# Performance work log

Measured on AMD Instinct MI355X. Metric: run time of the kernel, lower is better.

Reference implementation:

```python
import jax, jax.numpy as jnp
import numpy as np

EPS = 1e-5

def conv3x3(x, w, bias=None):
    y = jax.lax.conv_general_dilated(x, w, (1, 1), 'SAME',
                                     dimension_numbers=('NCHW', 'OIHW', 'NCHW'))
    if bias is not None:
        y = y + bias[None, :, None, None]
    return y

def batchnorm(x, g, b):
    m = x.mean((0, 2, 3), keepdims=True)
    v = x.var((0, 2, 3), keepdims=True)
    return (x - m) * jax.lax.rsqrt(v + EPS) * g[None, :, None, None] + b[None, :, None, None]

def deform_sample(x, offset, mask, dg=2):
    # x: [B,C,H,W]; offset: [B,dg*9*2,H,W] (dy,dx interleaved per mmcv); mask: [B,dg*9,H,W]
    B, C, H, W = x.shape
    K = 9
    cg = C // dg
    off = offset.reshape(B, dg, K, 2, H, W)
    dy, dx = off[:, :, :, 0], off[:, :, :, 1]
    m = mask.reshape(B, dg, K, H, W)
    ky = (jnp.repeat(jnp.arange(3), 3) - 1).astype(x.dtype)   # kernel row offset per tap
    kx = (jnp.tile(jnp.arange(3), 3) - 1).astype(x.dtype)     # kernel col offset per tap
    py = dy + jnp.arange(H, dtype=x.dtype)[None, None, None, :, None] + ky[None, None, :, None, None]
    px = dx + jnp.arange(W, dtype=x.dtype)[None, None, None, None, :] + kx[None, None, :, None, None]
    y0 = jnp.floor(py); x0 = jnp.floor(px)
    ly = py - y0; lx = px - x0
    y0i = y0.astype(jnp.int32); x0i = x0.astype(jnp.int32)
    y1i = y0i + 1; x1i = x0i + 1
    def ok(yy, xx):
        return ((yy >= 0) & (yy < H) & (xx >= 0) & (xx < W)).astype(x.dtype)
    xg = x.reshape(B, dg, cg, H * W)
    def gather(yy, xx):
        idx = (jnp.clip(yy, 0, H - 1) * W + jnp.clip(xx, 0, W - 1)).reshape(B, dg, -1)
        g = jax.vmap(jax.vmap(lambda im, ii: im[:, ii]))(xg, idx)   # [B,dg,cg,K*H*W]
        return g.reshape(B, dg, cg, K, H, W)
    w00 = ((1 - ly) * (1 - lx) * ok(y0i, x0i))[:, :, None]
    w01 = ((1 - ly) * lx * ok(y0i, x1i))[:, :, None]
    w10 = (ly * (1 - lx) * ok(y1i, x0i))[:, :, None]
    w11 = (ly * lx * ok(y1i, x1i))[:, :, None]
    val = (gather(y0i, x0i) * w00 + gather(y0i, x1i) * w01 +
           gather(y1i, x0i) * w10 + gather(y1i, x1i) * w11)
    return val * m[:, :, None]   # [B,dg,cg,K,H,W]

def reference(input_v, input_i, off_w, off_b, dconv_w, bn1_g, bn1_b, conv2_w, bn2_g, bn2_b):
    x = jnp.concatenate([input_v, input_i], axis=1)             # [B,C,H,W]
    off_all = conv3x3(x, off_w, off_b)                          # [B,54,H,W]
    o1, o2, mask = jnp.split(off_all, 3, axis=1)
    offset = jnp.concatenate([o1, o2], axis=1)                  # [B,36,H,W]
    mask = jax.nn.sigmoid(mask)                                 # [B,18,H,W]
    sampled = deform_sample(x, offset, mask, dg=2)              # [B,2,cg,9,H,W]
    O = dconv_w.shape[0]
    out = jnp.einsum('bgckhw,ogck->bohw', sampled, dconv_w.reshape(O, 2, -1, 9))
    out = jax.nn.relu(batchnorm(out, bn1_g, bn1_b))
    out = jax.nn.relu(batchnorm(conv3x3(out, conv2_w), bn2_g, bn2_b))
    return out

def setup_inputs() -> dict:
    key = jax.random.key(0)
    ks = jax.random.split(key, 8)
    B, Cm, O, H, W = 4, 128, 128, 64, 64
    C = 2 * Cm
    inp = {}
    inp['input_v'] = jax.random.normal(ks[0], (B, Cm, H, W), jnp.float32)
    inp['input_i'] = jax.random.normal(ks[1], (B, Cm, H, W), jnp.float32)
    # offset/mask conv (zero-init in torch; small random here for a non-trivial reference)
    inp['off_w'] = jax.random.normal(ks[2], (54, C, 3, 3), jnp.float32) * 0.02
    inp['off_b'] = jnp.zeros((54,), jnp.float32)
    inp['dconv_w'] = jax.random.normal(ks[3], (O, C, 3, 3), jnp.float32) * (1.0 / np.sqrt(C * 9))
    inp['bn1_g'] = jnp.ones((O,), jnp.float32)
    inp['bn1_b'] = jnp.zeros((O,), jnp.float32)
    inp['conv2_w'] = jax.random.normal(ks[4], (O, O, 3, 3), jnp.float32) * (1.0 / np.sqrt(O * 9))
    inp['bn2_g'] = jnp.ones((O,), jnp.float32)
    inp['bn2_b'] = jnp.zeros((O,), jnp.float32)
    return inp
```

## Files before the change

### kernel.cpp

```cpp
#include <hip/hip_runtime.h>

#define EPSBN 1e-5f

using s8v = __attribute__((ext_vector_type(8))) short;
using f4v = __attribute__((ext_vector_type(4))) float;

__device__ inline unsigned short f2bf(float f) {
  unsigned u = __float_as_uint(f);
  return (unsigned short)((u + 0x7FFFu + ((u >> 16) & 1u)) >> 16);
}
__device__ inline float bf2f(unsigned short h) {
  return __uint_as_float(((unsigned)h) << 16);
}

__global__ __launch_bounds__(256) void k_pack(const float* __restrict__ v, const float* __restrict__ im,
                                              unsigned short* __restrict__ xb) {
  __shared__ float tile[64][33];
  int b = blockIdx.z;
  int hw0 = blockIdx.x * 32;
  int c0 = blockIdx.y * 64;
  int tx = threadIdx.x, ty = threadIdx.y;
#pragma unroll
  for (int i = 0; i < 64; i += 8) {
    int c = c0 + ty + i;
    const float* src = (c < 128) ? (v + ((size_t)b * 128 + c) * 4096)
                                 : (im + ((size_t)b * 128 + (c - 128)) * 4096);
    tile[ty + i][tx] = src[hw0 + tx];
  }
  __syncthreads();
#pragma unroll
  for (int i = 0; i < 32; i += 8) {
    int hw = hw0 + ty + i;
    ushort2 o;
    o.x = f2bf(tile[2 * tx][ty + i]);
    o.y = f2bf(tile[2 * tx + 1][ty + i]);
    *(ushort2*)&xb[((size_t)(b * 4096 + hw)) * 256 + c0 + 2 * tx] = o;
  }
}

__global__ __launch_bounds__(256) void k_wprep_off(const float* __restrict__ w, unsigned short* __restrict__ wt) {
  int id = blockIdx.x * 256 + threadIdx.x;
  int lane = id & 63;
  int nb = (id >> 6) & 3;
  int ks = id >> 8;
  int ks2 = ks & 1, tap = (ks >> 1) % 9, cc = ks / 18;
  int o = nb * 16 + (lane & 15);
  int cb = cc * 64 + ks2 * 32 + ((lane >> 4) * 8);
  s8v r;
#pragma unroll
  for (int j = 0; j < 8; ++j) {
    float val = (o < 54) ? w[((size_t)o * 256 + cb + j) * 9 + tap] : 0.f;
    r[j] = (short)f2bf(val);
  }
  *(s8v*)&wt[(size_t)id * 8] = r;
}
__global__ __launch_bounds__(256) void k_wprep_d(const float* __restrict__ w, unsigned short* __restrict__ wt) {
  int id = blockIdx.x * 256 + threadIdx.x;
  int lane = id & 63;
  int nb = (id >> 6) & 7;
  int kstep = id >> 9;
  int chunk = kstep >> 2, ks4 = kstep & 3;
  int g = chunk / 9, kk = chunk % 9;
  int o = nb * 16 + (lane & 15);
  int cb = g * 128 + ks4 * 32 + ((lane >> 4) * 8);
  s8v r;
#pragma unroll
  for (int j = 0; j < 8; ++j) r[j] = (short)f2bf(w[((size_t)o * 256 + cb + j) * 9 + kk]);
  *(s8v*)&wt[(size_t)id * 8] = r;
}
__global__ __launch_bounds__(256) void k_wprep_2(const float* __restrict__ w, unsigned short* __restrict__ wt) {
  int id = blockIdx.x * 256 + threadIdx.x;
  int lane = id & 63;
  int nb = (id >> 6) & 7;
  int kstep = id >> 9;
  int ks2 = kstep & 1, tap = (kstep >> 1) % 9, cc = kstep / 18;
  int o = nb * 16 + (lane & 15);
  int cb = cc * 64 + ks2 * 32 + ((lane >> 4) * 8);
  s8v r;
#pragma unroll
  for (int j = 0; j < 8; ++j) r[j] = (short)f2bf(w[((size_t)o * 128 + cb + j) * 9 + tap]);
  *(s8v*)&wt[(size_t)id * 8] = r;
}

__global__ __launch_bounds__(512, 4) void k_offconv(const unsigned short* __restrict__ xb,
                                                    const unsigned short* __restrict__ wt,
                                                    const float* __restrict__ bias,
                                                    float* __restrict__ off) {
  __shared__ char Xs[102 * 512];
  int bid = blockIdx.x;
  int id8 = (bid & 7) * 64 + (bid >> 3);
  int w0 = (id8 & 1) * 32;
  int h = (id8 >> 1) & 63;
  int b = id8 >> 7;
  int t = threadIdx.x;
  int l = t & 63, wv = t >> 6;
  int pxg = wv >> 2, og = wv & 3;
  f4v acc = {0.f, 0.f, 0.f, 0.f};

  for (int id = t; id < 3264; id += 512) {
    int tr = id >> 5, oq8 = id & 31;
    int ky = tr / 34, col = tr % 34;
    int hh = h + ky - 1, ww = w0 + col - 1;
    s8v val = {0, 0, 0, 0, 0, 0, 0, 0};
    if ((unsigned)hh < 64u && (unsigned)ww < 64u)
      val = *(const s8v*)&xb[(((size_t)(b * 64 + hh)) * 64 + ww) * 256 + oq8 * 8];
    int byte = (tr * 512 + oq8 * 16) ^ ((tr & 7) << 4);
    *(s8v*)(Xs + byte) = val;
  }
  __syncthreads();
  int khi = l >> 4, lo = l & 15;
#pragma unroll
  for (int tap = 0; tap < 9; ++tap) {
    int ky = tap / 3, kx = tap % 3;
    int tr = ky * 34 + pxg * 16 + lo + kx;
#pragma unroll
    for (int ks8 = 0; ks8 < 8; ++ks8) {
      int rbyte = (tr * 512 + ks8 * 64 + khi * 16) ^ ((tr & 7) << 4);
      s8v a = *(const s8v*)(Xs + rbyte);
      int kstep = ((ks8 >> 1) * 9 + tap) * 2 + (ks8 & 1);
      s8v bfr = *(const s8v*)&wt[((size_t)(kstep * 4 + og) * 64 + l) * 8];
      acc = __builtin_amdgcn_mfma_f32_16x16x32_bf16(a, bfr, acc, 0, 0, 0);
    }
  }
  int o = og * 16 + lo;
  int pixb = (b * 64 + h) * 64 + w0;
  if (o < 54) {
    float bi = bias[o];
#pragma unroll
    for (int j = 0; j < 4; ++j) {
      int px = pixb + pxg * 16 + khi * 4 + j;
      float vv = acc[j] + bi;
      if (o >= 36) vv = 1.f / (1.f + __expf(-vv));
      off[(size_t)px * 54 + o] = vv;
    }
  }
}

#define DC_ISSUE(c, V, Q)                                   \
  do {                                                      \
    const unsigned* ip_ = sidx[(c)][px];                    \
    const float* qp_ = swt[(c)][px];                        \
    Q##0 = qp_[0]; Q##1 = qp_[1]; Q##2 = qp_[2]; Q##3 = qp_[3]; \
    V##0 = *(const s8v*)&xb[ip_[0] + chof];                 \
    V##1 = *(const s8v*)&xb[ip_[1] + chof];                 \
    V##2 = *(const s8v*)&xb[ip_[2] + chof];                 \
    V##3 = *(const s8v*)&xb[ip_[3] + chof];                 \
  } while (0)

#define DC_COMMIT(c, V, Q)                                  \
  do {                                                      \
    s8v r_;                                                 \
    _Pragma("unroll") for (int j_ = 0; j_ < 8; ++j_) {      \
      float f_ = Q##0 * bf2f((unsigned short)V##0[j_]) +    \
                 Q##1 * bf2f((unsigned short)V##1[j_]) +    \
                 Q##2 * bf2f((unsigned short)V##2[j_]) +    \
                 Q##3 * bf2f((unsigned short)V##3[j_]);     \
      r_[j_] = (short)f2bf(f_);                             \
    }                                                       \
    *(s8v*)(&At[(c) & 1][0] + wbyte) = r_;                  \
  } while (0)

__global__ __launch_bounds__(512, 4) void k_dconv(const unsigned short* __restrict__ xb,
                                                  const float* __restrict__ off,
                                                  const unsigned short* __restrict__ wt,
                                                  float* __restrict__ y1p,
                                                  float* __restrict__ st1, float* __restrict__ st2) {
  __shared__ unsigned int sidx[18][32][4];
  __shared__ float swt[18][32][4];
  __shared__ char At[2][8192];
  int t = threadIdx.x;
  int l = t & 63, wv = t >> 6;
  int pxg = wv >> 2, og = wv & 3;
  int bid = blockIdx.x;
  int id8 = (bid & 7) * 64 + (bid >> 3);
  int pixb = id8 * 32;
  int b = pixb >> 12, h = (pixb >> 6) & 63, w0 = pixb & 63;

  for (int id = t; id < 576; id += 512) {
    int chunk = id >> 5, ppx = id & 31;
    int g = chunk / 9, kk = chunk % 9;
    const float* op = off + (size_t)(pixb + ppx) * 54;
    float dy = op[(g * 9 + kk) * 2];
    float dx = op[(g * 9 + kk) * 2 + 1];
    float msk = op[36 + g * 9 + kk];
    float py = dy + (float)(h + kk / 3 - 1);
    float pxf = dx + (float)(w0 + ppx + kk % 3 - 1);
    float y0f = floorf(py), x0f = floorf(pxf);
    float ly = py - y0f, lx = pxf - x0f;
    int y0 = (int)y0f, x0 = (int)x0f;
    int y1 = y0 + 1, x1 = x0 + 1;
    float oky0 = (y0 >= 0 && y0 < 64) ? 1.f : 0.f;
    float oky1 = (y1 >= 0 && y1 < 64) ? 1.f : 0.f;
    float okx0 = (x0 >= 0 && x0 < 64) ? 1.f : 0.f;
    float okx1 = (x1 >= 0 && x1 < 64) ? 1.f : 0.f;
    int y0c = min(max(y0, 0), 63), y1c = min(max(y1, 0), 63);
    int x0c = min(max(x0, 0), 63), x1c = min(max(x1, 0), 63);
    unsigned base = (unsigned)(b * 4096);
    unsigned gofs = (unsigned)(g * 128);
    sidx[chunk][ppx][0] = (base + y0c * 64 + x0c) * 256u + gofs;
    sidx[chunk][ppx][1] = (base + y0c * 64 + x1c) * 256u + gofs;
    sidx[chunk][ppx][2] = (base + y1c * 64 + x0c) * 256u + gofs;
    sidx[chunk][ppx][3] = (base + y1c * 64 + x1c) * 256u + gofs;
    swt[chunk][ppx][0] = (1.f - ly) * (1.f - lx) * oky0 * okx0 * msk;
    swt[chunk][ppx][1] = (1.f - ly) * lx * oky0 * okx1 * msk;
    swt[chunk][ppx][2] = ly * (1.f - lx) * oky1 * okx0 * msk;
    swt[chunk][ppx][3] = ly * lx * oky1 * okx1 * msk;
  }
  __syncthreads();

  int px = t >> 4, oq = t & 15;
  unsigned chof = oq * 8u;
  int wbyte = (px * 256 + oq * 16) ^ ((px & 7) << 4);
  int khi = l >> 4, lo = l & 15;
  int trA = pxg * 16 + lo;

  s8v va0, va1, va2, va3, vb0, vb1, vb2, vb3;
  float qa0, qa1, qa2, qa3, qb0, qb1, qb2, qb3;

  DC_ISSUE(0, va, qa);
  DC_COMMIT(0, va, qa);
  DC_ISSUE(1, vb, qb);
  __syncthreads();

  f4v zero = {0.f, 0.f, 0.f, 0.f};
  f4v acc[2] = {zero, zero};

  for (int c = 0; c < 18; ++c) {
#pragma unroll
    for (int ks4 = 0; ks4 < 4; ++ks4) {
      int rbyte = (trA * 256 + ks4 * 64 + khi * 16) ^ ((trA & 7) << 4);
      s8v a = *(const s8v*)(&At[c & 1][0] + rbyte);
      int kstep = c * 4 + ks4;
#pragma unroll
      for (int nf = 0; nf < 2; ++nf) {
        s8v bfr = *(const s8v*)&wt[((size_t)(kstep * 8 + og * 2 + nf) * 64 + l) * 8];
        acc[nf] = __builtin_amdgcn_mfma_f32_16x16x32_bf16(a, bfr, acc[nf], 0, 0, 0);
      }
    }
    if (c < 17) {
      if ((c & 1) == 0) {
        if (c < 16) DC_ISSUE(c + 2, va, qa);
        DC_COMMIT(c + 1, vb, qb);
      } else {
        if (c < 16) DC_ISSUE(c + 2, vb, qb);
        DC_COMMIT(c + 1, va, qa);
      }
    }
    __syncthreads();
  }

  float s1v[2], s2v[2];
#pragma unroll
  for (int nf = 0; nf < 2; ++nf) {
    int o = og * 32 + nf * 16 + lo;
    s1v[nf] = 0.f; s2v[nf] = 0.f;
#pragma unroll
    for (int j = 0; j < 4; ++j) {
      float vv = acc[nf][j];
      y1p[(size_t)(pixb + pxg * 16 + khi * 4 + j) * 128 + o] = vv;
      s1v[nf] += vv; s2v[nf] += vv * vv;
    }
  }
  float* red = &swt[0][0][0];
  int r = pxg * 4 + khi;
#pragma unroll
  for (int nf = 0; nf < 2; ++nf) {
    int o = og * 32 + nf * 16 + lo;
    red[r * 128 + o] = s1v[nf];
    red[1024 + r * 128 + o] = s2v[nf];
  }
  __syncthreads();
  if (t < 128) {
    float a1 = 0.f, a2 = 0.f;
#pragma unroll
    for (int rr = 0; rr < 8; ++rr) { a1 += red[rr * 128 + t]; a2 += red[1024 + rr * 128 + t]; }
    atomicAdd(&st1[t], a1);
    atomicAdd(&st2[t], a2);
  }
}

__global__ __launch_bounds__(256) void k_bnrelu1(const float* __restrict__ yp, const float* __restrict__ s1,
                                                 const float* __restrict__ s2, const float* __restrict__ g,
                                                 const float* __restrict__ bb, unsigned short* __restrict__ yb) {
  __shared__ float sc[128], sh[128];
  int t = threadIdx.x;
  if (t < 128) {
    float m = s1[t] * (1.f / 16384.f);
    float var = s2[t] * (1.f / 16384.f) - m * m;
    float s = g[t] * rsqrtf(var + EPSBN);
    sc[t] = s;
    sh[t] = bb[t] - m * s;
  }
  __syncthreads();
  size_t i = ((size_t)blockIdx.x * 256 + t) * 8;
  int c0 = (int)(i & 127);
  float4 u = *(const float4*)&yp[i];
  float4 v = *(const float4*)&yp[i + 4];
  s8v r;
  r[0] = (short)f2bf(fmaxf(0.f, u.x * sc[c0 + 0] + sh[c0 + 0]));
  r[1] = (short)f2bf(fmaxf(0.f, u.y * sc[c0 + 1] + sh[c0 + 1]));
  r[2] = (short)f2bf(fmaxf(0.f, u.z * sc[c0 + 2] + sh[c0 + 2]));
  r[3] = (short)f2bf(fmaxf(0.f, u.w * sc[c0 + 3] + sh[c0 + 3]));
  r[4] = (short)f2bf(fmaxf(0.f, v.x * sc[c0 + 4] + sh[c0 + 4]));
  r[5] = (short)f2bf(fmaxf(0.f, v.y * sc[c0 + 5] + sh[c0 + 5]));
  r[6] = (short)f2bf(fmaxf(0.f, v.z * sc[c0 + 6] + sh[c0 + 6]));
  r[7] = (short)f2bf(fmaxf(0.f, v.w * sc[c0 + 7] + sh[c0 + 7]));
  *(s8v*)&yb[i] = r;
}

__global__ __launch_bounds__(512, 4) void k_conv2(const unsigned short* __restrict__ yb,
                                                  const unsigned short* __restrict__ wt,
                                                  float* __restrict__ y2p,
                                                  float* __restrict__ st1, float* __restrict__ st2) {
  __shared__ char Bs[102 * 256];
  int bid = blockIdx.x;
  int id8 = (bid & 7) * 64 + (bid >> 3);
  int w0 = (id8 & 1) * 32;
  int h = (id8 >> 1) & 63;
  int b = id8 >> 7;
  int t = threadIdx.x;
  int l = t & 63, wv = t >> 6;
  int pxg = wv >> 2, og = wv & 3;
  f4v zero = {0.f, 0.f, 0.f, 0.f};
  f4v acc[2] = {zero, zero};

  for (int id = t; id < 1632; id += 512) {
    int tr = id >> 4, oq = id & 15;
    int ky = tr / 34, col = tr % 34;
    int hh = h + ky - 1, ww = w0 + col - 1;
    s8v val = {0, 0, 0, 0, 0, 0, 0, 0};
    if ((unsigned)hh < 64u && (unsigned)ww < 64u)
      val = *(const s8v*)&yb[(((size_t)(b * 64 + hh)) * 64 + ww) * 128 + oq * 8];
    int byte = (tr * 256 + oq * 16) ^ ((tr & 7) << 4);
    *(s8v*)(Bs + byte) = val;
  }
  __syncthreads();
  int khi = l >> 4, lo = l & 15;
#pragma unroll
  for (int tap = 0; tap < 9; ++tap) {
    int ky = tap / 3, kx = tap % 3;
    int tr = ky * 34 + pxg * 16 + lo + kx;
#pragma unroll
    for (int ks4 = 0; ks4 < 4; ++ks4) {
      int rbyte = (tr * 256 + ks4 * 64 + khi * 16) ^ ((tr & 7) << 4);
      s8v a = *(const s8v*)(Bs + rbyte);
      int kstep = ((ks4 >> 1) * 9 + tap) * 2 + (ks4 & 1);
#pragma unroll
      for (int nf = 0; nf < 2; ++nf) {
        s8v bfr = *(const s8v*)&wt[((size_t)(kstep * 8 + og * 2 + nf) * 64 + l) * 8];
        acc[nf] = __builtin_amdgcn_mfma_f32_16x16x32_bf16(a, bfr, acc[nf], 0, 0, 0);
      }
    }
  }
  int pixb = (b * 64 + h) * 64 + w0;
  float s1v[2], s2v[2];
#pragma unroll
  for (int nf = 0; nf < 2; ++nf) {
    int o = og * 32 + nf * 16 + lo;
    s1v[nf] = 0.f; s2v[nf] = 0.f;
#pragma unroll
    for (int j = 0; j < 4; ++j) {
      float vv = acc[nf][j];
      y2p[(size_t)(pixb + pxg * 16 + khi * 4 + j) * 128 + o] = vv;
      s1v[nf] += vv; s2v[nf] += vv * vv;
    }
  }
  __syncthreads();
  float* red = (float*)Bs;
  int r = pxg * 4 + khi;
#pragma unroll
  for (int nf = 0; nf < 2; ++nf) {
    int o = og * 32 + nf * 16 + lo;
    red[r * 128 + o] = s1v[nf];
    red[1024 + r * 128 + o] = s2v[nf];
  }
  __syncthreads();
  if (t < 128) {
    float a1 = 0.f, a2 = 0.f;
#pragma unroll
    for (int rr = 0; rr < 8; ++rr) { a1 += red[rr * 128 + t]; a2 += red[1024 + rr * 128 + t]; }
    atomicAdd(&st1[t], a1);
    atomicAdd(&st2[t], a2);
  }
}

__global__ __launch_bounds__(256) void k_bnrelu2(const float* __restrict__ yp, const float* __restrict__ s1,
                                                 const float* __restrict__ s2, const float* __restrict__ g,
                                                 const float* __restrict__ bb, float* __restrict__ out) {
  __shared__ float sc[128], sh[128];
  int t = threadIdx.x;
  if (t < 128) {
    float m = s1[t] * (1.f / 16384.f);
    float var = s2[t] * (1.f / 16384.f) - m * m;
    float s = g[t] * rsqrtf(var + EPSBN);
    sc[t] = s;
    sh[t] = bb[t] - m * s;
  }
  __syncthreads();
  int bh = blockIdx.x;
  int b = bh >> 6, h = bh & 63;
  const float* src = yp + (size_t)bh * 64 * 128;
  for (int id = t; id < 64 * 128; id += 256) {
    int w = id & 63, o = id >> 6;
    float v = src[w * 128 + o];
    v = fmaxf(0.f, v * sc[o] + sh[o]);
    out[(((size_t)b * 128 + o) * 64 + h) * 64 + w] = v;
  }
}

extern "C" void kernel_launch(void* const* d_in, const int* in_sizes, int n_in,
                              void* d_out, int out_size, void* d_ws, size_t ws_size,
                              hipStream_t stream) {
  const float* in_v = (const float*)d_in[0];
  const float* in_i = (const float*)d_in[1];
  const float* off_w = (const float*)d_in[2];
  const float* off_b = (const float*)d_in[3];
  const float* dconv_w = (const float*)d_in[4];
  const float* bn1_g = (const float*)d_in[5];
  const float* bn1_b = (const float*)d_in[6];
  const float* conv2_w = (const float*)d_in[7];
  const float* bn2_g = (const float*)d_in[8];
  const float* bn2_b = (const float*)d_in[9];
  float* out = (float*)d_out;

  char* w = (char*)d_ws;
  unsigned short* xb = (unsigned short*)w;      w += (size_t)16384 * 256 * 2;
  float* off_nhwc = (float*)w;                  w += (size_t)16384 * 54 * 4;
  unsigned short* wtf_off = (unsigned short*)w; w += (size_t)18432 * 8 * 2;
  unsigned short* wtf_d = (unsigned short*)w;   w += (size_t)36864 * 8 * 2;
  unsigned short* wtf_2 = (unsigned short*)w;   w += (size_t)18432 * 8 * 2;
  float* y1p = (float*)w;                       w += (size_t)16384 * 128 * 4;
  unsigned short* y1b = (unsigned short*)w;     w += (size_t)16384 * 128 * 2;
  float* y2p = (float*)w;                       w += (size_t)16384 * 128 * 4;
  float* stats = (float*)w;                     w += 512 * 4;

  hipMemsetAsync(stats, 0, 512 * 4, stream);
  k_pack<<<dim3(128, 4, 4), dim3(32, 8), 0, stream>>>(in_v, in_i, xb);
  k_wprep_off<<<72, 256, 0, stream>>>(off_w, wtf_off);
  k_wprep_d<<<144, 256, 0, stream>>>(dconv_w, wtf_d);
  k_wprep_2<<<72, 256, 0, stream>>>(conv2_w, wtf_2);
  k_offconv<<<512, 512, 0, stream>>>(xb, wtf_off, off_b, off_nhwc);
  k_dconv<<<512, 512, 0, stream>>>(xb, off_nhwc, wtf_d, y1p, stats, stats + 128);
  k_bnrelu1<<<1024, 256, 0, stream>>>(y1p, stats, stats + 128, bn1_g, bn1_b, y1b);
  k_conv2<<<512, 512, 0, stream>>>(y1b, wtf_2, y2p, stats + 256, stats + 384);
  k_bnrelu2<<<256, 256, 0, stream>>>(y2p, stats + 256, stats + 384, bn2_g, bn2_b, out);
}
```

Measured before the change: 179.9 us.

## Remap MFMA wave tiling so each wave reuses its weight fragment across pixel tiles

In the dconv and conv2 kernels, each of the 8 waves now owns one 16-channel output group and both 16-pixel tiles. It loads the weight fragment once per k-step and reuses it for two MFMAs, where before it took one pixel tile and two output groups. The offset conv splits the reduction over input channels across two wave halves, reuses weights across both pixel tiles, and merges the partial sums through shared memory. The bilinear sample commit now uses a packed v_cvt_pk_bf16_f32 conversion, and launch-bounds occupancy drops from 4 to 3. The aim is to cut global weight-fragment loads and conversion instructions, at the cost of more LDS A-reads, an extra shared reduction and possibly lower occupancy.

```diff
diff --git a/kernel.cpp b/kernel.cpp
--- a/kernel.cpp
+++ b/kernel.cpp
@@ -82,11 +82,12 @@
   *(s8v*)&wt[(size_t)id * 8] = r;
 }
 
-__global__ __launch_bounds__(512, 4) void k_offconv(const unsigned short* __restrict__ xb,
+__global__ __launch_bounds__(512, 3) void k_offconv(const unsigned short* __restrict__ xb,
                                                     const unsigned short* __restrict__ wt,
                                                     const float* __restrict__ bias,
                                                     float* __restrict__ off) {
   __shared__ char Xs[102 * 512];
+  __shared__ float redx[2048];
   int bid = blockIdx.x;
   int id8 = (bid & 7) * 64 + (bid >> 3);
   int w0 = (id8 & 1) * 32;
@@ -94,8 +95,9 @@
   int b = id8 >> 7;
   int t = threadIdx.x;
   int l = t & 63, wv = t >> 6;
-  int pxg = wv >> 2, og = wv & 3;
-  f4v acc = {0.f, 0.f, 0.f, 0.f};
+  int og = wv & 3, kh = wv >> 2;
+  f4v zero = {0.f, 0.f, 0.f, 0.f};
+  f4v acc[2] = {zero, zero};
 
   for (int id = t; id < 3264; id += 512) {
     int tr = id >> 5, oq8 = id & 31;
@@ -112,26 +114,43 @@
 #pragma unroll
   for (int tap = 0; tap < 9; ++tap) {
     int ky = tap / 3, kx = tap % 3;
-    int tr = ky * 34 + pxg * 16 + lo + kx;
-#pragma unroll
-    for (int ks8 = 0; ks8 < 8; ++ks8) {
-      int rbyte = (tr * 512 + ks8 * 64 + khi * 16) ^ ((tr & 7) << 4);
-      s8v a = *(const s8v*)(Xs + rbyte);
-      int kstep = ((ks8 >> 1) * 9 + tap) * 2 + (ks8 & 1);
+#pragma unroll
+    for (int s = 0; s < 4; ++s) {
+      int cc = kh * 2 + (s >> 1);
+      int ks2 = s & 1;
+      int kstep = cc * 18 + tap * 2 + ks2;
+      int chb = cc * 128 + ks2 * 64 + khi * 16;
       s8v bfr = *(const s8v*)&wt[((size_t)(kstep * 4 + og) * 64 + l) * 8];
-      acc = __builtin_amdgcn_mfma_f32_16x16x32_bf16(a, bfr, acc, 0, 0, 0);
-    }
-  }
-  int o = og * 16 + lo;
-  int pixb = (b * 64 + h) * 64 + w0;
-  if (o < 54) {
-    float bi = bias[o];
-#pragma unroll
-    for (int j = 0; j < 4; ++j) {
-      int px = pixb + pxg * 16 + khi * 4 + j;
-      float vv = acc[j] + bi;
-      if (o >= 36) vv = 1.f / (1.f + __expf(-vv));
-      off[(size_t)px * 54 + o] = vv;
+#pragma unroll
+      for (int m = 0; m < 2; ++m) {
+        int tr = ky * 34 + m * 16 + lo + kx;
+        int rbyte = (tr * 512 + chb) ^ ((tr & 7) << 4);
+        s8v a = *(const s8v*)(Xs + rbyte);
+        acc[m] = __builtin_amdgcn_mfma_f32_16x16x32_bf16(a, bfr, acc[m], 0, 0, 0);
+      }
+    }
+  }
+  if (kh == 1) {
+#pragma unroll
+    for (int m = 0; m < 2; ++m)
+#pragma unroll
+      for (int j = 0; j < 4; ++j) redx[((og * 64 + l) * 2 + m) * 4 + j] = acc[m][j];
+  }
+  __syncthreads();
+  if (kh == 0) {
+    int o = og * 16 + lo;
+    int pixb = (b * 64 + h) * 64 + w0;
+    if (o < 54) {
+      float bi = bias[o];
+#pragma unroll
+      for (int m = 0; m < 2; ++m)
+#pragma unroll
+        for (int j = 0; j < 4; ++j) {
+          int px = pixb + m * 16 + khi * 4 + j;
+          float vv = acc[m][j] + redx[((og * 64 + l) * 2 + m) * 4 + j] + bi;
+          if (o >= 36) vv = 1.f / (1.f + __expf(-vv));
+          off[(size_t)px * 54 + o] = vv;
+        }
     }
   }
 }
@@ -149,18 +168,24 @@
 
 #define DC_COMMIT(c, V, Q)                                  \
   do {                                                      \
-    s8v r_;                                                 \
-    _Pragma("unroll") for (int j_ = 0; j_ < 8; ++j_) {      \
-      float f_ = Q##0 * bf2f((unsigned short)V##0[j_]) +    \
-                 Q##1 * bf2f((unsigned short)V##1[j_]) +    \
-                 Q##2 * bf2f((unsigned short)V##2[j_]) +    \
-                 Q##3 * bf2f((unsigned short)V##3[j_]);     \
-      r_[j_] = (short)f2bf(f_);                             \
+    unsigned rr_[4];                                        \
+    _Pragma("unroll") for (int jp_ = 0; jp_ < 4; ++jp_) {   \
+      float f0_ = Q##0 * bf2f((unsigned short)V##0[2 * jp_]) +     \
+                  Q##1 * bf2f((unsigned short)V##1[2 * jp_]) +     \
+                  Q##2 * bf2f((unsigned short)V##2[2 * jp_]) +     \
+                  Q##3 * bf2f((unsigned short)V##3[2 * jp_]);      \
+      float f1_ = Q##0 * bf2f((unsigned short)V##0[2 * jp_ + 1]) + \
+                  Q##1 * bf2f((unsigned short)V##1[2 * jp_ + 1]) + \
+                  Q##2 * bf2f((unsigned short)V##2[2 * jp_ + 1]) + \
+                  Q##3 * bf2f((unsigned short)V##3[2 * jp_ + 1]);  \
+      unsigned p_;                                          \
+      asm("v_cvt_pk_bf16_f32 %0, %1, %2" : "=v"(p_) : "v"(f0_), "v"(f1_)); \
+      rr_[jp_] = p_;                                        \
     }                                                       \
-    *(s8v*)(&At[(c) & 1][0] + wbyte) = r_;                  \
+    *(int4*)(&At[(c) & 1][0] + wbyte) = *(int4*)rr_;        \
   } while (0)
 
-__global__ __launch_bounds__(512, 4) void k_dconv(const unsigned short* __restrict__ xb,
+__global__ __launch_bounds__(512, 3) void k_dconv(const unsigned short* __restrict__ xb,
                                                   const float* __restrict__ off,
                                                   const unsigned short* __restrict__ wt,
                                                   float* __restrict__ y1p,
@@ -169,8 +194,7 @@
   __shared__ float swt[18][32][4];
   __shared__ char At[2][8192];
   int t = threadIdx.x;
-  int l = t & 63, wv = t >> 6;
-  int pxg = wv >> 2, og = wv & 3;
+  int l = t & 63, og = t >> 6;
   int bid = blockIdx.x;
   int id8 = (bid & 7) * 64 + (bid >> 3);
   int pixb = id8 * 32;
@@ -212,7 +236,6 @@
   unsigned chof = oq * 8u;
   int wbyte = (px * 256 + oq * 16) ^ ((px & 7) << 4);
   int khi = l >> 4, lo = l & 15;
-  int trA = pxg * 16 + lo;
 
   s8v va0, va1, va2, va3, vb0, vb1, vb2, vb3;
   float qa0, qa1, qa2, qa3, qb0, qb1, qb2, qb3;
@@ -228,13 +251,15 @@
   for (int c = 0; c < 18; ++c) {
 #pragma unroll
     for (int ks4 = 0; ks4 < 4; ++ks4) {
-      int rbyte = (trA * 256 + ks4 * 64 + khi * 16) ^ ((trA & 7) << 4);
-      s8v a = *(const s8v*)(&At[c & 1][0] + rbyte);
       int kstep = c * 4 + ks4;
-#pragma unroll
-      for (int nf = 0; nf < 2; ++nf) {
-        s8v bfr = *(const s8v*)&wt[((size_t)(kstep * 8 + og * 2 + nf) * 64 + l) * 8];
-        acc[nf] = __builtin_amdgcn_mfma_f32_16x16x32_bf16(a, bfr, acc[nf], 0, 0, 0);
+      s8v bfr = *(const s8v*)&wt[((size_t)(kstep * 8 + og) * 64 + l) * 8];
+      int chb = ks4 * 64 + khi * 16;
+#pragma unroll
+      for (int m = 0; m < 2; ++m) {
+        int trA = m * 16 + lo;
+        int rbyte = (trA * 256 + chb) ^ ((trA & 7) << 4);
+        s8v a = *(const s8v*)(&At[c & 1][0] + rbyte);
+        acc[m] = __builtin_amdgcn_mfma_f32_16x16x32_bf16(a, bfr, acc[m], 0, 0, 0);
       }
     }
     if (c < 17) {
@@ -249,31 +274,24 @@
     __syncthreads();
   }
 
-  float s1v[2], s2v[2];
-#pragma unroll
-  for (int nf = 0; nf < 2; ++nf) {
-    int o = og * 32 + nf * 16 + lo;
-    s1v[nf] = 0.f; s2v[nf] = 0.f;
+  int o = og * 16 + lo;
+  float s1v = 0.f, s2v = 0.f;
+#pragma unroll
+  for (int m = 0; m < 2; ++m)
 #pragma unroll
     for (int j = 0; j < 4; ++j) {
-      float vv = acc[nf][j];
-      y1p[(size_t)(pixb + pxg * 16 + khi * 4 + j) * 128 + o] = vv;
-      s1v[nf] += vv; s2v[nf] += vv * vv;
-    }
-  }
+      float vv = acc[m][j];
+      y1p[(size_t)(pixb + m * 16 + khi * 4 + j) * 128 + o] = vv;
+      s1v += vv; s2v += vv * vv;
+    }
   float* red = &swt[0][0][0];
-  int r = pxg * 4 + khi;
-#pragma unroll
-  for (int nf = 0; nf < 2; ++nf) {
-    int o = og * 32 + nf * 16 + lo;
-    red[r * 128 + o] = s1v[nf];
-    red[1024 + r * 128 + o] = s2v[nf];
-  }
+  red[khi * 128 + o] = s1v;
+  red[512 + khi * 128 + o] = s2v;
   __syncthreads();
   if (t < 128) {
     float a1 = 0.f, a2 = 0.f;
 #pragma unroll
-    for (int rr = 0; rr < 8; ++rr) { a1 += red[rr * 128 + t]; a2 += red[1024 + rr * 128 + t]; }
+    for (int rr = 0; rr < 4; ++rr) { a1 += red[rr * 128 + t]; a2 += red[512 + rr * 128 + t]; }
     atomicAdd(&st1[t], a1);
     atomicAdd(&st2[t], a2);
   }
@@ -308,7 +326,7 @@
   *(s8v*)&yb[i] = r;
 }
 
-__global__ __launch_bounds__(512, 4) void k_conv2(const unsigned short* __restrict__ yb,
+__global__ __launch_bounds__(512, 3) void k_conv2(const unsigned short* __restrict__ yb,
                                                   const unsigned short* __restrict__ wt,
                                                   float* __restrict__ y2p,
                                                   float* __restrict__ st1, float* __restrict__ st2) {
@@ -319,8 +337,7 @@
   int h = (id8 >> 1) & 63;
   int b = id8 >> 7;
   int t = threadIdx.x;
-  int l = t & 63, wv = t >> 6;
-  int pxg = wv >> 2, og = wv & 3;
+  int l = t & 63, og = t >> 6;
   f4v zero = {0.f, 0.f, 0.f, 0.f};
   f4v acc[2] = {zero, zero};
 
@@ -339,46 +356,40 @@
 #pragma unroll
   for (int tap = 0; tap < 9; ++tap) {
     int ky = tap / 3, kx = tap % 3;
-    int tr = ky * 34 + pxg * 16 + lo + kx;
 #pragma unroll
     for (int ks4 = 0; ks4 < 4; ++ks4) {
-      int rbyte = (tr * 256 + ks4 * 64 + khi * 16) ^ ((tr & 7) << 4);
-      s8v a = *(const s8v*)(Bs + rbyte);
       int kstep = ((ks4 >> 1) * 9 + tap) * 2 + (ks4 & 1);
-#pragma unroll
-      for (int nf = 0; nf < 2; ++nf) {
-        s8v bfr = *(const s8v*)&wt[((size_t)(kstep * 8 + og * 2 + nf) * 64 + l) * 8];
-        acc[nf] = __builtin_amdgcn_mfma_f32_16x16x32_bf16(a, bfr, acc[nf], 0, 0, 0);
+      s8v bfr = *(const s8v*)&wt[((size_t)(kstep * 8 + og) * 64 + l) * 8];
+      int chb = ks4 * 64 + khi * 16;
+#pragma unroll
+      for (int m = 0; m < 2; ++m) {
+        int tr = ky * 34 + m * 16 + lo + kx;
+        int rbyte = (tr * 256 + chb) ^ ((tr & 7) << 4);
+        s8v a = *(const s8v*)(Bs + rbyte);
+        acc[m] = __builtin_amdgcn_mfma_f32_16x16x32_bf16(a, bfr, acc[m], 0, 0, 0);
       }
     }
   }
+  __syncthreads();
   int pixb = (b * 64 + h) * 64 + w0;
-  float s1v[2], s2v[2];
-#pragma unroll
-  for (int nf = 0; nf < 2; ++nf) {
-    int o = og * 32 + nf * 16 + lo;
-    s1v[nf] = 0.f; s2v[nf] = 0.f;
+  int o = og * 16 + lo;
+  float s1v = 0.f, s2v = 0.f;
+#pragma unroll
+  for (int m = 0; m < 2; ++m)
 #pragma unroll
     for (int j = 0; j < 4; ++j) {
-      float vv = acc[nf][j];
-      y2p[(size_t)(pixb + pxg * 16 + khi * 4 + j) * 128 + o] = vv;
-      s1v[nf] += vv; s2v[nf] += vv * vv;
-    }
-  }
-  __syncthreads();
+      float vv = acc[m][j];
+      y2p[(size_t)(pixb + m * 16 + khi * 4 + j) * 128 + o] = vv;
+      s1v += vv; s2v += vv * vv;
+    }
   float* red = (float*)Bs;
-  int r = pxg * 4 + khi;
-#pragma unroll
-  for (int nf = 0; nf < 2; ++nf) {
-    int o = og * 32 + nf * 16 + lo;
-    red[r * 128 + o] = s1v[nf];
-    red[1024 + r * 128 + o] = s2v[nf];
-  }
+  red[khi * 128 + o] = s1v;
+  red[512 + khi * 128 + o] = s2v;
   __syncthreads();
   if (t < 128) {
     float a1 = 0.f, a2 = 0.f;
 #pragma unroll
-    for (int rr = 0; rr < 8; ++rr) { a1 += red[rr * 128 + t]; a2 += red[1024 + rr * 128 + t]; }
+    for (int rr = 0; rr < 4; ++rr) { a1 += red[rr * 128 + t]; a2 += red[512 + rr * 128 + t]; }
     atomicAdd(&st1[t], a1);
     atomicAdd(&st2[t], a2);
   }
```

After: 178.1 us. No clear change (-1.0%).
